# Kernel tuning notes

Hardware: AMD Instinct MI355X
Metric: run time of the kernel (lower is better)

The kernel has to match this reference:

```python
import jax, jax.numpy as jnp
import numpy as np

D = 256; HEADS = 8; DH = 32; LVLS = 3; PTS = 4; FF = 1024; FCD = 12544
SHAPES = ((100, 152), (50, 76), (25, 38))  # stride 8/16/32 maps for an 800x1216 image
INCH = (512, 1024, 2048)
N = 2; P_IMG = 1000


def sine_pos(h, w):
    # PositionEmbeddingSine, normalize=True, fully-valid mask
    eps = 1e-6; scale = 2.0 * np.pi
    y = jnp.cumsum(jnp.ones((h, w), jnp.float32), 0)
    x = jnp.cumsum(jnp.ones((h, w), jnp.float32), 1)
    y = y / (y[-1:, :] + eps) * scale
    x = x / (x[:, -1:] + eps) * scale
    dim_t = 10000.0 ** ((2.0 * (jnp.arange(128) // 2)).astype(jnp.float32) / 128.0)
    def inter(p):  # interleave sin/cos like torch.stack(...).flatten(3)
        return jnp.stack([jnp.sin(p[..., 0::2]), jnp.cos(p[..., 1::2])], -1).reshape(h, w, 128)
    return jnp.concatenate([inter(y[..., None] / dim_t), inter(x[..., None] / dim_t)], -1).reshape(h * w, D)


def bilinear(img, gx, gy):
    # F.grid_sample bilinear, align_corners=False, padding_mode='zeros'
    # img [C,H,W]; gx,gy in [-1,1] of any shape -> out [C, *gx.shape]
    C, H, W = img.shape
    x = ((gx + 1.0) * W - 1.0) * 0.5
    y = ((gy + 1.0) * H - 1.0) * 0.5
    x0 = jnp.floor(x); y0 = jnp.floor(y)
    wx = x - x0; wy = y - y0
    x0i = x0.astype(jnp.int32); y0i = y0.astype(jnp.int32)
    def g(xi, yi):
        ok = ((xi >= 0) & (xi < W) & (yi >= 0) & (yi < H)).astype(img.dtype)
        v = img[:, jnp.clip(yi, 0, H - 1), jnp.clip(xi, 0, W - 1)]
        return v * ok[None]
    return (g(x0i, y0i) * ((1 - wx) * (1 - wy))[None]
            + g(x0i + 1, y0i) * (wx * (1 - wy))[None]
            + g(x0i, y0i + 1) * ((1 - wx) * wy)[None]
            + g(x0i + 1, y0i + 1) * (wx * wy)[None])


def layernorm(x, g, b):
    mu = x.mean(-1, keepdims=True)
    var = ((x - mu) ** 2).mean(-1, keepdims=True)
    return (x - mu) / jnp.sqrt(var + 1e-5) * g + b


def _forward(feat0, feat1, feat2, point_coords, projw, projb, gng, gnb, level_embed,
             w_off, b_off, w_attn, b_attn, w_val, b_val, w_out, b_out,
             ln1_g, ln1_b, ln2_g, ln2_b, w_ff1, b_ff1, w_ff2, b_ff2, fc_w, fc_b):
    feats = (feat0, feat1, feat2)
    srcs = []; poss = []
    for l in range(LVLS):
        # input_proj: 1x1 conv + GroupNorm(32, 256)
        s = jnp.einsum('nchw,oc->nohw', feats[l], projw[l]) + projb[l][None, :, None, None]
        n, c, h, w = s.shape
        sg = s.reshape(n, 32, c // 32, h, w)
        mu = sg.mean((2, 3, 4), keepdims=True)
        var = ((sg - mu) ** 2).mean((2, 3, 4), keepdims=True)
        s = ((sg - mu) / jnp.sqrt(var + 1e-5)).reshape(n, c, h, w) * gng[l][None, :, None, None] + gnb[l][None, :, None, None]
        srcs.append(s.reshape(n, c, h * w).transpose(0, 2, 1))
        poss.append(sine_pos(h, w)[None] + level_embed[l][None, None, :])
    src = jnp.concatenate(srcs, 1)            # [N, Len, D]
    pos = jnp.concatenate(poss, 1)            # [1, Len, D] broadcast
    # reference points (valid_ratios == 1)
    refs = []
    for (h, w) in SHAPES:
        gy, gx = jnp.meshgrid((jnp.arange(h) + 0.5) / h, (jnp.arange(w) + 0.5) / w, indexing='ij')
        refs.append(jnp.stack([gx.ravel(), gy.ravel()], -1))
    ref = jnp.concatenate(refs, 0)            # [Len, 2] (x, y)
    Lq = src.shape[1]
    q = src + pos
    value = (src @ w_val.T + b_val).reshape(N, Lq, HEADS, DH)
    off = (q @ w_off.T + b_off).reshape(N, Lq, HEADS, LVLS, PTS, 2)
    aw = jax.nn.softmax((q @ w_attn.T + b_attn).reshape(N, Lq, HEADS, LVLS * PTS), -1).reshape(N, Lq, HEADS, LVLS, PTS)
    norm = jnp.array([[w, h] for (h, w) in SHAPES], jnp.float32)  # [L, 2] offset normalizer (W_, H_)
    locs = ref[None, :, None, None, None, :] + off / norm[None, None, None, :, None, :]  # [N,Lq,H,L,P,2]
    # MSDeformAttn core: per-level bilinear gather, accumulate weighted samples
    acc = jnp.zeros((N * HEADS, DH, Lq), src.dtype)
    start = 0
    for lvl, (h, w) in enumerate(SHAPES):
        v = value[:, start:start + h * w].transpose(0, 2, 3, 1).reshape(N * HEADS, DH, h, w)
        g = (2.0 * locs[:, :, :, lvl] - 1.0).transpose(0, 2, 1, 3, 4).reshape(N * HEADS, Lq, PTS, 2)
        s = jax.vmap(bilinear)(v, g[..., 0], g[..., 1])                 # [NH, DH, Lq, PTS]
        a = aw[:, :, :, lvl].transpose(0, 2, 1, 3).reshape(N * HEADS, 1, Lq, PTS)
        acc = acc + (s * a).sum(-1)
        start += h * w
    attn_out = acc.reshape(N, HEADS * DH, Lq).transpose(0, 2, 1) @ w_out.T + b_out
    x = layernorm(src + attn_out, ln1_g, ln1_b)
    ff = jax.nn.relu(x @ w_ff1.T + b_ff1) @ w_ff2.T + b_ff2
    x = layernorm(x + ff, ln2_g, ln2_b)
    # take level-0 tokens back to a feature map
    H0, W0 = SHAPES[0]
    mem = x.transpose(0, 2, 1)[:, :, :H0 * W0].reshape(N, D, H0, W0)
    # point_sample: grid_sample at 2*coords-1
    gpc = 2.0 * point_coords - 1.0
    pf = jax.vmap(bilinear)(mem, gpc[..., 0], gpc[..., 1])              # [N, D, P]
    pf = pf.transpose(0, 2, 1).reshape(N * P_IMG, D)
    # fc: Conv1d(256 -> 12544, k=1) + relu, then squeeze/permute
    return jax.nn.relu(pf @ fc_w.T + fc_b[None])


def setup_inputs() -> dict:
    key = jax.random.key(0)
    ki = iter(jax.random.split(key, 48))
    def rn(shape, scale):
        return jax.random.normal(next(ki), shape, jnp.float32) * scale
    d = {}
    d['feat0'] = jax.random.normal(next(ki), (N, 512, 100, 152), jnp.float32)
    d['feat1'] = jax.random.normal(next(ki), (N, 1024, 50, 76), jnp.float32)
    d['feat2'] = jax.random.normal(next(ki), (N, 2048, 25, 38), jnp.float32)
    d['point_coords'] = jax.random.uniform(next(ki), (N, P_IMG, 2), jnp.float32)
    d['gt_classes'] = jax.random.randint(next(ki), (N * P_IMG,), 0, 81)
    for l in range(LVLS):
        cin = INCH[l]
        d[f'proj{l}_w'] = rn((D, cin), 1.0 / np.sqrt(cin))
        d[f'proj{l}_b'] = jnp.zeros((D,), jnp.float32)
        d[f'gn{l}_g'] = jnp.ones((D,), jnp.float32)
        d[f'gn{l}_b'] = jnp.zeros((D,), jnp.float32)
    d['level_embed'] = rn((LVLS, D), 1.0)
    d['w_off'] = rn((HEADS * LVLS * PTS * 2, D), 0.01)
    d['b_off'] = rn((HEADS * LVLS * PTS * 2,), 0.2)
    d['w_attn'] = rn((HEADS * LVLS * PTS, D), 0.01)
    d['b_attn'] = jnp.zeros((HEADS * LVLS * PTS,), jnp.float32)
    d['w_val'] = rn((D, D), 1.0 / 16)
    d['b_val'] = jnp.zeros((D,), jnp.float32)
    d['w_out'] = rn((D, D), 1.0 / 16)
    d['b_out'] = jnp.zeros((D,), jnp.float32)
    d['ln1_g'] = jnp.ones((D,), jnp.float32); d['ln1_b'] = jnp.zeros((D,), jnp.float32)
    d['ln2_g'] = jnp.ones((D,), jnp.float32); d['ln2_b'] = jnp.zeros((D,), jnp.float32)
    d['w_ff1'] = rn((FF, D), 1.0 / 16); d['b_ff1'] = jnp.zeros((FF,), jnp.float32)
    d['w_ff2'] = rn((D, FF), 1.0 / 32); d['b_ff2'] = jnp.zeros((D,), jnp.float32)
    d['fc_w'] = rn((FCD, D), 1.0 / 16); d['fc_b'] = jnp.zeros((FCD,), jnp.float32)
    return d


def reference(feat0, feat1, feat2, point_coords, gt_classes,
              proj0_w, proj0_b, gn0_g, gn0_b, proj1_w, proj1_b, gn1_g, gn1_b,
              proj2_w, proj2_b, gn2_g, gn2_b, level_embed,
              w_off, b_off, w_attn, b_attn, w_val, b_val, w_out, b_out,
              ln1_g, ln1_b, ln2_g, ln2_b, w_ff1, b_ff1, w_ff2, b_ff2, fc_w, fc_b):
    out = _forward(feat0, feat1, feat2, point_coords,
                   (proj0_w, proj1_w, proj2_w), (proj0_b, proj1_b, proj2_b),
                   (gn0_g, gn1_g, gn2_g), (gn0_b, gn1_b, gn2_b), level_embed,
                   w_off, b_off, w_attn, b_attn, w_val, b_val, w_out, b_out,
                   ln1_g, ln1_b, ln2_g, ln2_b, w_ff1, b_ff1, w_ff2, b_ff2, fc_w, fc_b)
    return (out, gt_classes)
```

## Files before the change

### kernel.cpp

```cpp
#include <hip/hip_runtime.h>
#include <cstddef>
#include <cstdint>

#define D_MODEL 256
#define LQ 19950
#define NBATCH 2
#define NT (NBATCH*LQ)

typedef short  bf16x8 __attribute__((ext_vector_type(8)));
typedef float  f32x4  __attribute__((ext_vector_type(4)));
typedef unsigned short u16x8 __attribute__((ext_vector_type(8)));
typedef unsigned short u16x4 __attribute__((ext_vector_type(4)));
typedef _Float16 h16x2 __attribute__((ext_vector_type(2)));

__device__ __forceinline__ unsigned short f2b(float f) {
  unsigned u = __float_as_uint(f);
  u += 0x7fff + ((u >> 16) & 1);
  return (unsigned short)(u >> 16);
}
__device__ __forceinline__ float b2f(unsigned short s) {
  return __uint_as_float(((unsigned)s) << 16);
}
__device__ __forceinline__ bf16x8 pack8(float4 a, float4 b) {
  bf16x8 r;
  r[0]=(short)f2b(a.x); r[1]=(short)f2b(a.y); r[2]=(short)f2b(a.z); r[3]=(short)f2b(a.w);
  r[4]=(short)f2b(b.x); r[5]=(short)f2b(b.y); r[6]=(short)f2b(b.z); r[7]=(short)f2b(b.w);
  return r;
}

#if __has_builtin(__builtin_amdgcn_global_load_lds)
#define HAVE_GLL 1
__device__ __forceinline__ void gload16(const void* g, void* lds_base_uniform) {
  __builtin_amdgcn_global_load_lds(
      (const __attribute__((address_space(1))) void*)g,
      (__attribute__((address_space(3))) void*)lds_base_uniform, 16, 0, 0);
}
#else
#define HAVE_GLL 0
#endif

template<bool ABF, int BMODE, bool CBF, bool RELU, bool ROWBIAS>
__global__ __launch_bounds__(256) void mgemm(
    const void* __restrict__ Av, const void* __restrict__ Bv,
    const float* __restrict__ bias, void* __restrict__ Cv,
    int M, int N, int K, int lda, int ldb, long sB, long sC, int zShift)
{
  __shared__ unsigned short As[64][72];
  __shared__ unsigned short Bs[64][72];
  const int tid = threadIdx.x;
  const int n0 = blockIdx.x * 64, m0 = blockIdx.y * 64;
  const int zb = blockIdx.z;
  const int n_b = zb >> zShift;
  const int kBase = (zb & ((1 << zShift) - 1)) * K;
  const int lane = tid & 63;
  const int wave = tid >> 6;
  const int l15 = lane & 15, q = lane >> 4;
  const int m_off = (wave >> 1) * 32, n_off = (wave & 1) * 32;
  f32x4 acc[2][2] = {};

  for (int k0 = kBase; k0 < kBase + K; k0 += 64) {
    {
      int row = tid >> 2, kc = (tid & 3) * 8;
      int gm = m0 + row;
      bf16x8 v0 = (bf16x8)0, v1 = (bf16x8)0;
      if (gm < M) {
        if constexpr (ABF) {
          const unsigned short* A = (const unsigned short*)Av;
          v0 = *(const bf16x8*)&A[(size_t)gm*lda + k0 + kc];
          v1 = *(const bf16x8*)&A[(size_t)gm*lda + k0 + kc + 32];
        } else {
          const float* A = (const float*)Av;
          const float* p = &A[(size_t)gm*lda + k0 + kc];
          v0 = pack8(*(const float4*)p,      *(const float4*)(p+4));
          v1 = pack8(*(const float4*)(p+32), *(const float4*)(p+36));
        }
      }
      *(bf16x8*)&As[row][kc]    = v0;
      *(bf16x8*)&As[row][kc+32] = v1;
    }
    if constexpr (BMODE == 1) {
      const float* Bp = (const float*)Bv + (size_t)n_b * sB;
      int kr = tid >> 3, nc = (tid & 7) * 8;
      #pragma unroll
      for (int half = 0; half < 2; ++half) {
        int kk = kr + half*32;
        const float* p = &Bp[(size_t)(k0+kk)*ldb + n0 + nc];
        float v[8];
        if (n0 + nc + 7 < N) {
          float2 a0 = *(const float2*)p,     a1 = *(const float2*)(p+2);
          float2 a2 = *(const float2*)(p+4), a3 = *(const float2*)(p+6);
          v[0]=a0.x; v[1]=a0.y; v[2]=a1.x; v[3]=a1.y;
          v[4]=a2.x; v[5]=a2.y; v[6]=a3.x; v[7]=a3.y;
        } else {
          #pragma unroll
          for (int i=0;i<8;++i) v[i] = (n0+nc+i < N) ? p[i] : 0.f;
        }
        #pragma unroll
        for (int i=0;i<8;++i) Bs[nc+i][kk] = f2b(v[i]);
      }
    }
    __syncthreads();
    #pragma unroll
    for (int s = 0; s < 2; ++s) {
      bf16x8 a0 = *(const bf16x8*)&As[m_off      + l15][s*32 + q*8];
      bf16x8 a1 = *(const bf16x8*)&As[m_off + 16 + l15][s*32 + q*8];
      bf16x8 b0 = *(const bf16x8*)&Bs[n_off      + l15][s*32 + q*8];
      bf16x8 b1 = *(const bf16x8*)&Bs[n_off + 16 + l15][s*32 + q*8];
      acc[0][0] = __builtin_amdgcn_mfma_f32_16x16x32_bf16(a0, b0, acc[0][0], 0,0,0);
      acc[0][1] = __builtin_amdgcn_mfma_f32_16x16x32_bf16(a0, b1, acc[0][1], 0,0,0);
      acc[1][0] = __builtin_amdgcn_mfma_f32_16x16x32_bf16(a1, b0, acc[1][0], 0,0,0);
      acc[1][1] = __builtin_amdgcn_mfma_f32_16x16x32_bf16(a1, b1, acc[1][1], 0,0,0);
    }
    __syncthreads();
  }
  float* Cf = (float*)Cv + (size_t)zb * sC;
  unsigned short* Cb = (unsigned short*)Cv + (size_t)zb * sC;
  #pragma unroll
  for (int r = 0; r < 2; ++r) {
    #pragma unroll
    for (int c = 0; c < 2; ++c) {
      #pragma unroll
      for (int v = 0; v < 4; ++v) {
        int gm = m0 + m_off + r*16 + q*4 + v;
        int gn = n0 + n_off + c*16 + l15;
        if (gm < M && gn < N) {
          float o = acc[r][c][v];
          if (bias) o += ROWBIAS ? bias[gm] : bias[gn];
          if (RELU) o = fmaxf(o, 0.f);
          if constexpr (CBF) Cb[(size_t)gm*N + gn] = f2b(o);
          else               Cf[(size_t)gm*N + gn] = o;
        }
      }
    }
  }
}

__global__ __launch_bounds__(256) void proj_reduce2(
    const float* __restrict__ part, const float* __restrict__ bias,
    float* __restrict__ out, int HW, int S)
{
  int half = HW >> 1;
  int per_n = D_MODEL * half;
  int total = NBATCH * per_n;
  const float2* p2 = (const float2*)part;
  float2* o2 = (float2*)out;
  for (int i = blockIdx.x*256 + threadIdx.x; i < total; i += gridDim.x*256) {
    int n = i / per_n;
    int r = i - n*per_n;
    int o = r / half;
    int hw2 = r - o*half;
    float ax = 0.f, ay = 0.f;
    for (int s = 0; s < S; ++s) {
      float2 v = p2[((size_t)(n*S+s)*D_MODEL + o)*half + hw2];
      ax += v.x; ay += v.y;
    }
    float b = bias[o];
    o2[(size_t)o*HW + (size_t)n*half + hw2] = make_float2(ax+b, ay+b);
  }
}

template<bool CBF, bool RELU, bool RB>
__global__ __launch_bounds__(512) void gemm_bb(
    const unsigned short* __restrict__ A, const unsigned short* __restrict__ B,
    const float* __restrict__ bias, void* __restrict__ Cv,
    int M, int N, int K, int lda, int ldb)
{
  __shared__ unsigned short SA[8192];
  __shared__ unsigned short SB[8192];
  const int tid = threadIdx.x;
  const int lane = tid & 63, wave = tid >> 6;
  const int nwg = gridDim.x * gridDim.y;
  const int flat = blockIdx.y * gridDim.x + blockIdx.x;
  const int qn = nwg >> 3, rr = nwg & 7;
  const int xcd = flat & 7, lid = flat >> 3;
  const int swz = (xcd < rr ? xcd*(qn+1) : rr*(qn+1) + (xcd-rr)*qn) + lid;
  const int n0 = (swz % gridDim.x) * 128;
  const int m0 = (swz / gridDim.x) * 128;

  const int l15 = lane & 15, q = lane >> 4;
  const int m_off = (wave >> 2) * 64, n_off = (wave & 3) * 32;
  const int sr = lane >> 3;
  const int ssl = (lane & 7) ^ sr;
  const int rs = l15 & 7;
  f32x4 acc[4][2] = {};

  for (int k0 = 0; k0 < K; k0 += 64) {
    #pragma unroll
    for (int c = 0; c < 2; ++c) {
      int ch = wave*2 + c;
      const unsigned short* ga = A + (size_t)(m0 + ch*8 + sr)*lda + k0 + ssl*8;
      const unsigned short* gb = B + (size_t)(n0 + ch*8 + sr)*ldb + k0 + ssl*8;
#if HAVE_GLL
      gload16(ga, &SA[ch*512]);
      gload16(gb, &SB[ch*512]);
#else
      *(bf16x8*)&SA[ch*512 + lane*8] = *(const bf16x8*)ga;
      *(bf16x8*)&SB[ch*512 + lane*8] = *(const bf16x8*)gb;
#endif
    }
    __syncthreads();
    #pragma unroll
    for (int s = 0; s < 2; ++s) {
      int ps = ((s*4 + q) ^ rs) * 8;
      bf16x8 af[4], bfr[2];
      #pragma unroll
      for (int i = 0; i < 4; ++i)
        af[i] = *(const bf16x8*)&SA[(m_off + i*16 + l15)*64 + ps];
      #pragma unroll
      for (int j = 0; j < 2; ++j)
        bfr[j] = *(const bf16x8*)&SB[(n_off + j*16 + l15)*64 + ps];
      #pragma unroll
      for (int i = 0; i < 4; ++i)
        #pragma unroll
        for (int j = 0; j < 2; ++j)
          acc[i][j] = __builtin_amdgcn_mfma_f32_16x16x32_bf16(af[i], bfr[j], acc[i][j], 0,0,0);
    }
    __syncthreads();
  }

  float* Cf = (float*)Cv;
  unsigned short* Cb = (unsigned short*)Cv;
  #pragma unroll
  for (int i = 0; i < 4; ++i) {
    #pragma unroll
    for (int j = 0; j < 2; ++j) {
      #pragma unroll
      for (int v = 0; v < 4; ++v) {
        int gm = m0 + m_off + i*16 + q*4 + v;
        int gn = n0 + n_off + j*16 + l15;
        if (gm < M && gn < N) {
          float o = acc[i][j][v];
          if (bias) o += RB ? bias[gm] : bias[gn];
          if (RELU) o = fmaxf(o, 0.f);
          if constexpr (CBF) Cb[(size_t)gm*N + gn] = f2b(o);
          else               Cf[(size_t)gm*N + gn] = o;
        }
      }
    }
  }
}

template<bool CBF, bool RELU, bool RB>
__global__ __launch_bounds__(512) void gemm_wide(
    const unsigned short* __restrict__ A, const unsigned short* __restrict__ B,
    const float* __restrict__ bias, void* __restrict__ Cv,
    int M, int N, int K, int lda, int ldb)
{
  __shared__ unsigned short SA[8192];
  __shared__ unsigned short SB[16384];
  const int tid = threadIdx.x;
  const int lane = tid & 63, wave = tid >> 6;
  const int nwg = gridDim.x * gridDim.y;
  const int flat = blockIdx.y * gridDim.x + blockIdx.x;
  const int qn = nwg >> 3, rr = nwg & 7;
  const int xcd = flat & 7, lid = flat >> 3;
  const int swz = (xcd < rr ? xcd*(qn+1) : rr*(qn+1) + (xcd-rr)*qn) + lid;
  const int n0 = (swz % gridDim.x) * 256;
  const int m0 = (swz / gridDim.x) * 128;

  const int l15 = lane & 15, q = lane >> 4;
  const int m_off = (wave >> 2) * 64, n_off = (wave & 3) * 64;
  const int sr = lane >> 3;
  const int ssl = (lane & 7) ^ sr;
  const int rs = l15 & 7;
  f32x4 acc[4][4] = {};

  for (int k0 = 0; k0 < K; k0 += 64) {
    #pragma unroll
    for (int c = 0; c < 2; ++c) {
      int ch = wave*2 + c;
      const unsigned short* ga = A + (size_t)(m0 + ch*8 + sr)*lda + k0 + ssl*8;
#if HAVE_GLL
      gload16(ga, &SA[ch*512]);
#else
      *(bf16x8*)&SA[ch*512 + lane*8] = *(const bf16x8*)ga;
#endif
    }
    #pragma unroll
    for (int c = 0; c < 4; ++c) {
      int ch = wave*4 + c;
      const unsigned short* gb = B + (size_t)(n0 + ch*8 + sr)*ldb + k0 + ssl*8;
#if HAVE_GLL
      gload16(gb, &SB[ch*512]);
#else
      *(bf16x8*)&SB[ch*512 + lane*8] = *(const bf16x8*)gb;
#endif
    }
    __syncthreads();
    #pragma unroll
    for (int s = 0; s < 2; ++s) {
      int ps = ((s*4 + q) ^ rs) * 8;
      bf16x8 af[4], bfr[4];
      #pragma unroll
      for (int i = 0; i < 4; ++i)
        af[i] = *(const bf16x8*)&SA[(m_off + i*16 + l15)*64 + ps];
      #pragma unroll
      for (int j = 0; j < 4; ++j)
        bfr[j] = *(const bf16x8*)&SB[(n_off + j*16 + l15)*64 + ps];
      #pragma unroll
      for (int i = 0; i < 4; ++i)
        #pragma unroll
        for (int j = 0; j < 4; ++j)
          acc[i][j] = __builtin_amdgcn_mfma_f32_16x16x32_bf16(af[i], bfr[j], acc[i][j], 0,0,0);
    }
    __syncthreads();
  }

  float* Cf = (float*)Cv;
  unsigned short* Cb = (unsigned short*)Cv;
  #pragma unroll
  for (int i = 0; i < 4; ++i) {
    #pragma unroll
    for (int j = 0; j < 4; ++j) {
      #pragma unroll
      for (int v = 0; v < 4; ++v) {
        int gm = m0 + m_off + i*16 + q*4 + v;
        int gn = n0 + n_off + j*16 + l15;
        if (gm < M && gn < N) {
          float o = acc[i][j][v];
          if (bias) o += RB ? bias[gm] : bias[gn];
          if (RELU) o = fmaxf(o, 0.f);
          if constexpr (CBF) Cb[(size_t)gm*N + gn] = f2b(o);
          else               Cf[(size_t)gm*N + gn] = o;
        }
      }
    }
  }
}

__global__ __launch_bounds__(512) void gemm_vo(
    const unsigned short* __restrict__ Asrc, const unsigned short* __restrict__ Aq,
    const unsigned short* __restrict__ Bv,   const unsigned short* __restrict__ Bo,
    const float* __restrict__ bias_v, const float* __restrict__ bias_o,
    unsigned short* __restrict__ Cv, unsigned short* __restrict__ Co, int M)
{
  __shared__ unsigned short SA[8192];
  __shared__ unsigned short SB[8192];
  const int tid = threadIdx.x;
  const int lane = tid & 63, wave = tid >> 6;
  const int nwg = gridDim.x * gridDim.y;
  const int flat = blockIdx.y * gridDim.x + blockIdx.x;
  const int qn = nwg >> 3, rr = nwg & 7;
  const int xcd = flat & 7, lid = flat >> 3;
  const int swz = (xcd < rr ? xcd*(qn+1) : rr*(qn+1) + (xcd-rr)*qn) + lid;
  const int colid = swz % gridDim.x;
  const int m0 = (swz / gridDim.x) * 128;

  const unsigned short* A; const unsigned short* B;
  const float* bias; unsigned short* C; int N, n0; bool isv;
  if (colid < 2) { A = Asrc; B = Bv; bias = bias_v; C = Cv; N = 256; n0 = colid*128; isv = true; }
  else           { A = Aq;   B = Bo; bias = bias_o; C = Co; N = 288; n0 = (colid-2)*128; isv = false; }

  const int l15 = lane & 15, q = lane >> 4;
  const int m_off = (wave >> 2) * 64, n_off = (wave & 3) * 32;
  const int sr = lane >> 3;
  const int ssl = (lane & 7) ^ sr;
  const int rs = l15 & 7;
  f32x4 acc[4][2] = {};

  for (int k0 = 0; k0 < 256; k0 += 64) {
    #pragma unroll
    for (int c = 0; c < 2; ++c) {
      int ch = wave*2 + c;
      const unsigned short* ga = A + (size_t)(m0 + ch*8 + sr)*256 + k0 + ssl*8;
      const unsigned short* gb = B + (size_t)(n0 + ch*8 + sr)*256 + k0 + ssl*8;
#if HAVE_GLL
      gload16(ga, &SA[ch*512]);
      gload16(gb, &SB[ch*512]);
#else
      *(bf16x8*)&SA[ch*512 + lane*8] = *(const bf16x8*)ga;
      *(bf16x8*)&SB[ch*512 + lane*8] = *(const bf16x8*)gb;
#endif
    }
    __syncthreads();
    #pragma unroll
    for (int s = 0; s < 2; ++s) {
      int ps = ((s*4 + q) ^ rs) * 8;
      bf16x8 af[4], bfr[2];
      #pragma unroll
      for (int i = 0; i < 4; ++i)
        af[i] = *(const bf16x8*)&SA[(m_off + i*16 + l15)*64 + ps];
      #pragma unroll
      for (int j = 0; j < 2; ++j)
        bfr[j] = *(const bf16x8*)&SB[(n_off + j*16 + l15)*64 + ps];
      #pragma unroll
      for (int i = 0; i < 4; ++i)
        #pragma unroll
        for (int j = 0; j < 2; ++j)
          acc[i][j] = __builtin_amdgcn_mfma_f32_16x16x32_bf16(af[i], bfr[j], acc[i][j], 0,0,0);
    }
    __syncthreads();
  }

  #pragma unroll
  for (int i = 0; i < 4; ++i) {
    #pragma unroll
    for (int j = 0; j < 2; ++j) {
      #pragma unroll
      for (int v = 0; v < 4; ++v) {
        int gm = m0 + m_off + i*16 + q*4 + v;
        int gn = n0 + n_off + j*16 + l15;
        if (gm < M && gn < N) {
          float o = acc[i][j][v] + bias[gn];
          unsigned short bits;
          if (isv) { _Float16 hh = (_Float16)o; bits = *(unsigned short*)&hh; }
          else     { bits = f2b(o); }
          C[(size_t)gm*N + gn] = bits;
        }
      }
    }
  }
}

__global__ __launch_bounds__(256) void tconv(
    const float* __restrict__ feat, unsigned short* __restrict__ featT,
    int C, int HW)
{
  __shared__ float T[32][33];
  int hw0 = blockIdx.x*32, c0 = blockIdx.y*32, n = blockIdx.z;
  const float* base = feat + (size_t)n*C*HW;
  int tx = threadIdx.x & 31, ty = threadIdx.x >> 5;
  #pragma unroll
  for (int it=0; it<4; ++it) {
    int c = c0 + ty + it*8;
    int hw = hw0 + tx;
    T[ty+it*8][tx] = (hw < HW) ? base[(size_t)c*HW + hw] : 0.f;
  }
  __syncthreads();
  #pragma unroll
  for (int it=0; it<4; ++it) {
    int tl = ty + it*8;
    int tok = hw0 + tl;
    if (tok < HW) {
      featT[((size_t)n*HW + tok)*C + c0 + tx] = f2b(T[tx][tl]);
    }
  }
}

struct W9 { const float* src[9]; unsigned short* dst[9]; int nv[9]; };
__global__ __launch_bounds__(256) void wconv(W9 w)
{
  int s = blockIdx.y;
  const float4* src = (const float4*)w.src[s];
  unsigned short* dst = w.dst[s];
  int n = w.nv[s];
  for (int i = blockIdx.x*256 + threadIdx.x; i < n; i += gridDim.x*256) {
    float4 v = src[i];
    u16x4 o = { f2b(v.x), f2b(v.y), f2b(v.z), f2b(v.w) };
    *(u16x4*)(dst + (size_t)i*4) = o;
  }
}

__global__ __launch_bounds__(288) void biascat(
    const float* __restrict__ b_off, const float* __restrict__ b_attn,
    float* __restrict__ out)
{
  int i = threadIdx.x;
  out[i] = (i < 192) ? b_off[i] : b_attn[i - 192];
}

__global__ __launch_bounds__(256) void gn_partial2(
    const float* __restrict__ s2, float* __restrict__ partials, int HW)
{
  int g = blockIdx.x, n = blockIdx.y, c = blockIdx.z;
  int NHW = HW*2;
  int nvec2 = HW >> 1;
  int total = nvec2*8;
  float sum = 0.f, sq = 0.f;
  for (int j = c*256 + threadIdx.x; j < total; j += 2048) {
    int r = j / nvec2;
    int v = j - r*nvec2;
    const float2 x = *(const float2*)(s2 + (size_t)(g*8+r)*NHW + (size_t)n*HW + v*2);
    sum += x.x + x.y;
    sq  += x.x*x.x + x.y*x.y;
  }
  #pragma unroll
  for (int m=32;m;m>>=1){ sum += __shfl_xor(sum,m,64); sq += __shfl_xor(sq,m,64); }
  __shared__ float s1[4], s2s[4];
  int w = threadIdx.x >> 6;
  if ((threadIdx.x & 63) == 0) { s1[w]=sum; s2s[w]=sq; }
  __syncthreads();
  if (threadIdx.x == 0) {
    partials[(((size_t)n*32+g)*8 + c)*2]     = s1[0]+s1[1]+s1[2]+s1[3];
    partials[(((size_t)n*32+g)*8 + c)*2 + 1] = s2s[0]+s2s[1]+s2s[2]+s2s[3];
  }
}

__global__ __launch_bounds__(256) void gn_apply2(
    const float* __restrict__ s2, const float* __restrict__ partials,
    const float* __restrict__ gw, const float* __restrict__ gb,
    const float* __restrict__ le,
    float* __restrict__ src, unsigned short* __restrict__ srcbf,
    unsigned short* __restrict__ qb,
    int HW, int loff, int W, float invW, float invH2pi, float invW2pi)
{
  __shared__ float T[32][33];
  __shared__ float smu[4], srs[4];
  int tx = threadIdx.x & 31, ty = threadIdx.x >> 5;
  int hw0 = blockIdx.x*32, o0 = blockIdx.y*32, n = blockIdx.z;
  int NHW = HW*2;
  if (threadIdx.x < 4) {
    int g = (o0 >> 3) + threadIdx.x;
    float S = 0.f, Q = 0.f;
    #pragma unroll
    for (int c = 0; c < 8; ++c) {
      S += partials[(((size_t)n*32+g)*8 + c)*2];
      Q += partials[(((size_t)n*32+g)*8 + c)*2 + 1];
    }
    float inv = 1.f/(float)(8*HW);
    float mu = S*inv;
    float var = Q*inv - mu*mu;
    smu[threadIdx.x] = mu;
    srs[threadIdx.x] = rsqrtf(var + 1e-5f);
  }
  __syncthreads();
  #pragma unroll
  for (int it=0; it<4; ++it) {
    int ol = ty + it*8;
    int o = o0 + ol;
    int hw = hw0 + tx;
    float v = 0.f;
    if (hw < HW) {
      v = (s2[(size_t)o*NHW + (size_t)n*HW + hw] - smu[ol>>3])*srs[ol>>3]*gw[o] + gb[o];
    }
    T[ol][tx] = v;
  }
  __syncthreads();
  int d = o0 + tx;
  int m = (d & 127) >> 1;
  float invt = __expf((float)m * -0.14391156516f);
  float lev  = le[d];
  #pragma unroll
  for (int it=0; it<4; ++it) {
    int tl = ty + it*8;
    int tok = hw0 + tl;
    if (tok < HW) {
      size_t idx = ((size_t)n*LQ + loff + tok)*D_MODEL + d;
      float v = T[tx][tl];
      src[idx] = v;
      srcbf[idx] = f2b(v);
      int i = __float2int_rd(((float)tok + 0.5f) * invW);
      int j = tok - i*W;
      float ang = ((d < 128) ? (float)(i+1)*invH2pi : (float)(j+1)*invW2pi) * invt;
      float pe = (d & 1) ? __cosf(ang) : __sinf(ang);
      qb[idx] = f2b(v + pe + lev);
    }
  }
}

__global__ __launch_bounds__(256) void deform_sample(
    const unsigned short* __restrict__ value, const unsigned short* __restrict__ offaw,
    unsigned short* __restrict__ accb)
{
  int idx = blockIdx.x*256 + threadIdx.x;
  if (idx >= NT*8*4) return;
  int quarter = idx & 3;
  int h = (idx >> 2) & 7;
  int row = idx >> 5;
  int n = (row >= LQ) ? 1 : 0;
  int tok = row - n*LQ;

  float bxs0, bxs1, bxs2, bys0, bys1, bys2;
  if (tok < 15200) {
    int ti = tok/152, tj = tok - ti*152;
    float bx = tj + 0.5f, by = ti + 0.5f;
    bxs0 = bx - 0.5f;         bys0 = by - 0.5f;
    bxs1 = bx*0.5f - 0.5f;    bys1 = by*0.5f - 0.5f;
    bxs2 = bx*0.25f - 0.5f;   bys2 = by*0.25f - 0.5f;
  } else if (tok < 19000) {
    int hw = tok - 15200; int ti = hw/76, tj = hw - ti*76;
    float bx = tj + 0.5f, by = ti + 0.5f;
    bxs0 = bx*2.f - 0.5f;     bys0 = by*2.f - 0.5f;
    bxs1 = bx - 0.5f;         bys1 = by - 0.5f;
    bxs2 = bx*0.5f - 0.5f;    bys2 = by*0.5f - 0.5f;
  } else {
    int hw = tok - 19000; int ti = hw/38, tj = hw - ti*38;
    float bx = tj + 0.5f, by = ti + 0.5f;
    bxs0 = bx*4.f - 0.5f;     bys0 = by*4.f - 0.5f;
    bxs1 = bx*2.f - 0.5f;     bys1 = by*2.f - 0.5f;
    bxs2 = bx - 0.5f;         bys2 = by - 0.5f;
  }
  const float bxs[3] = {bxs0, bxs1, bxs2};
  const float bys[3] = {bys0, bys1, bys2};

  const unsigned short* offr = offaw + (size_t)row*288 + h*24;
  const unsigned short* awr  = offaw + (size_t)row*288 + 192 + h*12;
  float off[24];
  {
    u16x8 o0 = *(const u16x8*)offr;
    u16x8 o1 = *(const u16x8*)(offr+8);
    u16x8 o2 = *(const u16x8*)(offr+16);
    #pragma unroll
    for (int c=0;c<8;++c){ off[c]=b2f(o0[c]); off[8+c]=b2f(o1[c]); off[16+c]=b2f(o2[c]); }
  }
  float lg[12];
  {
    u16x4 a0 = *(const u16x4*)awr;
    u16x4 a1 = *(const u16x4*)(awr+4);
    u16x4 a2 = *(const u16x4*)(awr+8);
    #pragma unroll
    for (int c=0;c<4;++c){ lg[c]=b2f(a0[c]); lg[4+c]=b2f(a1[c]); lg[8+c]=b2f(a2[c]); }
  }
  float mx = -1e30f;
  #pragma unroll
  for (int i=0;i<12;++i) mx = fmaxf(mx, lg[i]);
  float ssum = 0.f;
  #pragma unroll
  for (int i=0;i<12;++i){ lg[i] = __expf(lg[i]-mx); ssum += lg[i]; }
  float sinv = 1.f/ssum;

  h16x2 acc2[4] = {};
  const int HH[3]={100,50,25}, WW[3]={152,76,38}, OO[3]={0,15200,19000};
  int chbase = h*32 + quarter*8;
  const _Float16* vhalf = (const _Float16*)value;
  #pragma unroll
  for (int lvl=0; lvl<3; ++lvl) {
    const int H=HH[lvl], W=WW[lvl], lo=OO[lvl];
    const _Float16* vbase = vhalf + ((size_t)(n*LQ + lo)*D_MODEL) + chbase;
    #pragma unroll
    for (int p=0; p<4; ++p) {
      float ox = off[lvl*8 + p*2];
      float oy = off[lvl*8 + p*2 + 1];
      float a  = lg[lvl*4 + p] * sinv;
      float x = bxs[lvl] + ox;
      float y = bys[lvl] + oy;
      float x0f = floorf(x), y0f = floorf(y);
      float wx = x - x0f, wy = y - y0f;
      int x0 = (int)x0f, y0 = (int)y0f;
      float w00 = (1.f-wx)*(1.f-wy)*a, w10 = wx*(1.f-wy)*a;
      float w01 = (1.f-wx)*wy*a,       w11 = wx*wy*a;
      if ((unsigned)x0 < (unsigned)(W-1) && (unsigned)y0 < (unsigned)(H-1)) {
        const h16x2* p00 = (const h16x2*)(vbase + (size_t)(y0*W + x0)*D_MODEL);
        const h16x2* p10 = (const h16x2*)(vbase + (size_t)(y0*W + x0 + 1)*D_MODEL);
        const h16x2* p01 = (const h16x2*)(vbase + (size_t)((y0+1)*W + x0)*D_MODEL);
        const h16x2* p11 = (const h16x2*)(vbase + (size_t)((y0+1)*W + x0 + 1)*D_MODEL);
        _Float16 h00 = (_Float16)w00, h10 = (_Float16)w10;
        _Float16 h01 = (_Float16)w01, h11 = (_Float16)w11;
        h16x2 wp00 = {h00,h00}, wp10 = {h10,h10}, wp01 = {h01,h01}, wp11 = {h11,h11};
        #pragma unroll
        for (int k=0;k<4;++k) {
          acc2[k] += wp00*p00[k];
          acc2[k] += wp10*p10[k];
          acc2[k] += wp01*p01[k];
          acc2[k] += wp11*p11[k];
        }
      } else {
        float tw[4] = { w00, w10, w01, w11 };
        #pragma unroll
        for (int t=0; t<4; ++t) {
          int xi = x0 + (t & 1), yi = y0 + (t >> 1);
          if (xi >= 0 && xi < W && yi >= 0 && yi < H) {
            _Float16 wh = (_Float16)tw[t];
            h16x2 wp = {wh, wh};
            const h16x2* vr = (const h16x2*)(vbase + (size_t)(yi*W + xi)*D_MODEL);
            #pragma unroll
            for (int k=0;k<4;++k) acc2[k] += wp*vr[k];
          }
        }
      }
    }
  }
  unsigned short* o = accb + (size_t)row*D_MODEL + chbase;
  u16x8 ov;
  #pragma unroll
  for (int k=0;k<4;++k) {
    ov[k*2]   = f2b((float)acc2[k][0]);
    ov[k*2+1] = f2b((float)acc2[k][1]);
  }
  *(u16x8*)o = ov;
}

template<bool EMITBF>
__global__ __launch_bounds__(256) void ln_add(
    const float* __restrict__ A, const float* __restrict__ B,
    const float* __restrict__ g, const float* __restrict__ b,
    float* __restrict__ out, unsigned short* __restrict__ outbf, int rows)
{
  int wid = (blockIdx.x * 256 + threadIdx.x) >> 6;
  int lane = threadIdx.x & 63;
  if (wid >= rows) return;
  size_t base = (size_t)wid * D_MODEL;
  float4 va = *(const float4*)&A[base + lane*4];
  float4 vb = *(const float4*)&B[base + lane*4];
  float v[4] = {va.x+vb.x, va.y+vb.y, va.z+vb.z, va.w+vb.w};
  float s = v[0]+v[1]+v[2]+v[3];
  #pragma unroll
  for (int m=32; m; m>>=1) s += __shfl_xor(s, m, 64);
  float mu = s * (1.f/256.f);
  float qq = 0.f;
  #pragma unroll
  for (int i=0;i<4;++i){ float d=v[i]-mu; qq += d*d; }
  #pragma unroll
  for (int m=32; m; m>>=1) qq += __shfl_xor(qq, m, 64);
  float rstd = rsqrtf(qq*(1.f/256.f) + 1e-5f);
  float o[4];
  #pragma unroll
  for (int i=0;i<4;++i){
    int d = lane*4+i;
    o[i] = (v[i]-mu)*rstd*g[d] + b[d];
  }
  *(float4*)&out[base + lane*4] = make_float4(o[0],o[1],o[2],o[3]);
  if constexpr (EMITBF) {
    u16x4 ob = { f2b(o[0]), f2b(o[1]), f2b(o[2]), f2b(o[3]) };
    *(u16x4*)&outbf[base + lane*4] = ob;
  }
}

__global__ __launch_bounds__(256) void point_sample(
    const float* __restrict__ x2, const float* __restrict__ pc,
    unsigned short* __restrict__ pf)
{
  int pidx = blockIdx.x;
  int n = pidx / 1000;
  float px = pc[(size_t)pidx*2], py = pc[(size_t)pidx*2+1];
  float x = ((2.f*px)*152.f - 1.f)*0.5f;
  float y = ((2.f*py)*100.f - 1.f)*0.5f;
  float x0f=floorf(x), y0f=floorf(y);
  float wx=x-x0f, wy=y-y0f;
  int x0=(int)x0f, y0=(int)y0f;
  int d = threadIdx.x;
  float accv = 0.f;
  #pragma unroll
  for (int t=0;t<4;++t) {
    int xi = x0 + (t&1), yi = y0 + (t>>1);
    float w = ((t&1)?wx:(1.f-wx)) * ((t>>1)?wy:(1.f-wy));
    if (xi>=0 && xi<152 && yi>=0 && yi<100) {
      accv += w * x2[((size_t)(n*LQ + yi*152 + xi))*D_MODEL + d];
    }
  }
  pf[(size_t)pidx*D_MODEL + d] = f2b(accv);
}

__global__ void copy_gt(const int* __restrict__ gt, float* __restrict__ out, int nels)
{
  int i = blockIdx.x*256 + threadIdx.x;
  if (i < nels) out[i] = (float)gt[i];
}

extern "C" void kernel_launch(void* const* d_in, const int* in_sizes, int n_in,
                              void* d_out, int out_size, void* d_ws, size_t ws_size,
                              hipStream_t stream)
{
  const float* feat[3]  = {(const float*)d_in[0], (const float*)d_in[1], (const float*)d_in[2]};
  const float* pc       = (const float*)d_in[3];
  const int*   gt       = (const int*)d_in[4];
  const float* projw[3] = {(const float*)d_in[5],  (const float*)d_in[9],  (const float*)d_in[13]};
  const float* projb[3] = {(const float*)d_in[6],  (const float*)d_in[10], (const float*)d_in[14]};
  const float* gng[3]   = {(const float*)d_in[7],  (const float*)d_in[11], (const float*)d_in[15]};
  const float* gnb[3]   = {(const float*)d_in[8],  (const float*)d_in[12], (const float*)d_in[16]};
  const float* level_embed = (const float*)d_in[17];
  const float* w_off  = (const float*)d_in[18];
  const float* b_off  = (const float*)d_in[19];
  const float* w_attn = (const float*)d_in[20];
  const float* b_attn = (const float*)d_in[21];
  const float* w_val  = (const float*)d_in[22];
  const float* b_val  = (const float*)d_in[23];
  const float* w_out  = (const float*)d_in[24];
  const float* b_out  = (const float*)d_in[25];
  const float* ln1g   = (const float*)d_in[26];
  const float* ln1b   = (const float*)d_in[27];
  const float* ln2g   = (const float*)d_in[28];
  const float* ln2b   = (const float*)d_in[29];
  const float* wff1   = (const float*)d_in[30];
  const float* bff1   = (const float*)d_in[31];
  const float* wff2   = (const float*)d_in[32];
  const float* bff2   = (const float*)d_in[33];
  const float* fcw    = (const float*)d_in[34];
  const float* fcb    = (const float*)d_in[35];

  float* ws    = (float*)d_ws;
  float* s_tmp = ws;
  unsigned short* q_b     = (unsigned short*)(s_tmp + 10214400);
  unsigned short* value_b = q_b + 10214400;
  float* srcb  = (float*)(value_b + 10214400);
  float* xreg  = srcb + 10214400;
  unsigned short* offaw   = (unsigned short*)(xreg + 10214400);
  unsigned short* wbf     = offaw + 11491200;
  float* partials = (float*)(wbf + 4333568);
  float* boffaw   = partials + 1024;

  unsigned short* wv_bf  = wbf;
  unsigned short* wof_bf = wbf + 65536;
  unsigned short* wat_bf = wbf + 114688;
  unsigned short* wou_bf = wbf + 139264;
  unsigned short* wf1_bf = wbf + 204800;
  unsigned short* wf2_bf = wbf + 466944;
  unsigned short* wfc_bf = wbf + 729088;
  unsigned short* wp0_bf = wbf + 3940352;
  unsigned short* wp1_bf = wbf + 4071424;

  unsigned short* featT = q_b;
  float* kpart = (float*)offaw;
  unsigned short* src_bf = (unsigned short*)xreg;
  unsigned short* acc_b = q_b;
  unsigned short* xb_bf = offaw;
  unsigned short* hbuf  = (unsigned short*)s_tmp;
  unsigned short* pf    = value_b;
  float* ybuf = srcb;
  float* x2   = s_tmp;

  W9 w9;
  w9.src[0]=w_val;    w9.dst[0]=wv_bf;  w9.nv[0]=65536/4;
  w9.src[1]=w_off;    w9.dst[1]=wof_bf; w9.nv[1]=49152/4;
  w9.src[2]=w_attn;   w9.dst[2]=wat_bf; w9.nv[2]=24576/4;
  w9.src[3]=w_out;    w9.dst[3]=wou_bf; w9.nv[3]=65536/4;
  w9.src[4]=wff1;     w9.dst[4]=wf1_bf; w9.nv[4]=262144/4;
  w9.src[5]=wff2;     w9.dst[5]=wf2_bf; w9.nv[5]=262144/4;
  w9.src[6]=fcw;      w9.dst[6]=wfc_bf; w9.nv[6]=3211264/4;
  w9.src[7]=projw[0]; w9.dst[7]=wp0_bf; w9.nv[7]=131072/4;
  w9.src[8]=projw[1]; w9.dst[8]=wp1_bf; w9.nv[8]=262144/4;
  wconv<<<dim3(512, 9), 256, 0, stream>>>(w9);
  biascat<<<1, 288, 0, stream>>>(b_off, b_attn, boffaw);

  const float PI2 = 6.28318530717958647692f;
  {
    tconv<<<dim3(475, 16, 2), 256, 0, stream>>>(feat[0], featT, 512, 15200);
    gemm_wide<false,false,true><<<dim3(119, 2), 512, 0, stream>>>(
        wp0_bf, featT, projb[0], s_tmp, 256, 30400, 512, 512, 512);
    gn_partial2<<<dim3(32, 2, 8), 256, 0, stream>>>(s_tmp, partials, 15200);
    gn_apply2<<<dim3(475, 8, 2), 256, 0, stream>>>(
        s_tmp, partials, gng[0], gnb[0], level_embed, srcb, src_bf, q_b,
        15200, 0, 152, 1.0f/152.f, PI2/(100.f+1e-6f), PI2/(152.f+1e-6f));
  }
  {
    tconv<<<dim3(119, 32, 2), 256, 0, stream>>>(feat[1], featT, 1024, 3800);
    gemm_wide<false,false,true><<<dim3(30, 2), 512, 0, stream>>>(
        wp1_bf, featT, projb[1], s_tmp, 256, 7600, 1024, 1024, 1024);
    gn_partial2<<<dim3(32, 2, 8), 256, 0, stream>>>(s_tmp, partials, 3800);
    gn_apply2<<<dim3(119, 8, 2), 256, 0, stream>>>(
        s_tmp, partials, gng[1], gnb[1], level_embed + 256, srcb, src_bf, q_b,
        3800, 15200, 76, 1.0f/76.f, PI2/(50.f+1e-6f), PI2/(76.f+1e-6f));
  }
  {
    mgemm<false,1,false,false,true><<<dim3(15, 4, 8), 256, 0, stream>>>(
        projw[2], feat[2], nullptr, kpart, D_MODEL, 950, 512, 2048, 950,
        (long)2048*950, (long)D_MODEL*950, 2);
    int total2 = NBATCH * D_MODEL * (950 >> 1);
    int gr = (total2 + 255) / 256; if (gr > 2048) gr = 2048;
    proj_reduce2<<<gr, 256, 0, stream>>>(kpart, projb[2], s_tmp, 950, 4);
    gn_partial2<<<dim3(32, 2, 8), 256, 0, stream>>>(s_tmp, partials, 950);
    gn_apply2<<<dim3(30, 8, 2), 256, 0, stream>>>(
        s_tmp, partials, gng[2], gnb[2], level_embed + 512, srcb, src_bf, q_b,
        950, 19000, 38, 1.0f/38.f, PI2/(25.f+1e-6f), PI2/(38.f+1e-6f));
  }

  int gm128 = (NT + 127) / 128;
  gemm_vo<<<dim3(5, gm128), 512, 0, stream>>>(
      src_bf, q_b, wv_bf, wof_bf, b_val, boffaw, value_b, offaw, NT);

  deform_sample<<<(NT*8*4 + 255)/256, 256, 0, stream>>>(value_b, offaw, acc_b);

  gemm_bb<false,false,false><<<dim3(2, gm128), 512, 0, stream>>>(
      acc_b, wou_bf, b_out, s_tmp, NT, 256, 256, 256, 256);
  ln_add<true><<<(NT+3)/4, 256, 0, stream>>>(srcb, s_tmp, ln1g, ln1b, xreg, xb_bf, NT);

  gemm_wide<true,true,false><<<dim3(4, gm128), 512, 0, stream>>>(
      xb_bf, wf1_bf, bff1, hbuf, NT, 1024, 256, 256, 256);
  gemm_bb<false,false,false><<<dim3(2, gm128), 512, 0, stream>>>(
      hbuf, wf2_bf, bff2, ybuf, NT, 256, 1024, 1024, 1024);

  ln_add<false><<<(NT+3)/4, 256, 0, stream>>>(xreg, ybuf, ln2g, ln2b, x2, nullptr, NT);

  point_sample<<<2000, 256, 0, stream>>>(x2, pc, pf);
  gemm_wide<false,true,false><<<dim3(49, (2000+127)/128), 512, 0, stream>>>(
      pf, wfc_bf, fcb, (float*)d_out, 2000, 12544, 256, 256, 256);
  copy_gt<<<8, 256, 0, stream>>>(gt, (float*)d_out + (size_t)2000*12544, 2000);
}
```

Measured before the change: 480.7 us.

## Fuse residual add and LayerNorm into full-width output GEMM epilogues

Replaces the generic wide GEMM with a 128x256-tile GEMM whose tile covers the whole 256-wide model row. Its epilogue adds bias and the residual, reduces row mean and variance through shuffles and shared memory, and writes the normalized output, optionally also in bf16. This removes the two separate ln_add kernels and the fp32 intermediate round trips for the out-projection and FF2 results. The other former wide-GEMM calls now use gemm_bb with doubled grid x, and buffer aliasing is adjusted. Variance is computed as E[x^2]-mu^2, which is slightly less numerically stable, and the fused kernel launches only one block column, so there is less parallelism per GEMM.

After: 525.8 us. +9.4%, slower.

```diff
diff --git a/kernel.cpp b/kernel.cpp
--- a/kernel.cpp
+++ b/kernel.cpp
@@ -240,29 +240,30 @@
   }
 }
 
-template<bool CBF, bool RELU, bool RB>
-__global__ __launch_bounds__(512) void gemm_wide(
+template<bool EMITBF>
+__global__ __launch_bounds__(512) void gemm_ln(
     const unsigned short* __restrict__ A, const unsigned short* __restrict__ B,
-    const float* __restrict__ bias, void* __restrict__ Cv,
-    int M, int N, int K, int lda, int ldb)
+    const float* __restrict__ bias, const float* __restrict__ R,
+    const float* __restrict__ g, const float* __restrict__ b,
+    float* __restrict__ out, unsigned short* __restrict__ outbf,
+    int M, int K, int lda, int ldb)
 {
   __shared__ unsigned short SA[8192];
   __shared__ unsigned short SB[16384];
   const int tid = threadIdx.x;
   const int lane = tid & 63, wave = tid >> 6;
-  const int nwg = gridDim.x * gridDim.y;
-  const int flat = blockIdx.y * gridDim.x + blockIdx.x;
-  const int qn = nwg >> 3, rr = nwg & 7;
+  const int nwg = gridDim.y;
+  const int flat = blockIdx.y;
+  const int qn = nwg >> 3, rrm = nwg & 7;
   const int xcd = flat & 7, lid = flat >> 3;
-  const int swz = (xcd < rr ? xcd*(qn+1) : rr*(qn+1) + (xcd-rr)*qn) + lid;
-  const int n0 = (swz % gridDim.x) * 256;
-  const int m0 = (swz / gridDim.x) * 128;
+  const int swz = (xcd < rrm ? xcd*(qn+1) : rrm*(qn+1) + (xcd-rrm)*qn) + lid;
+  const int m0 = swz * 128;
 
   const int l15 = lane & 15, q = lane >> 4;
   const int m_off = (wave >> 2) * 64, n_off = (wave & 3) * 64;
   const int sr = lane >> 3;
   const int ssl = (lane & 7) ^ sr;
-  const int rs = l15 & 7;
+  const int rsk = l15 & 7;
   f32x4 acc[4][4] = {};
 
   for (int k0 = 0; k0 < K; k0 += 64) {
@@ -279,7 +280,7 @@
     #pragma unroll
     for (int c = 0; c < 4; ++c) {
       int ch = wave*4 + c;
-      const unsigned short* gb = B + (size_t)(n0 + ch*8 + sr)*ldb + k0 + ssl*8;
+      const unsigned short* gb = B + (size_t)(ch*8 + sr)*ldb + k0 + ssl*8;
 #if HAVE_GLL
       gload16(gb, &SB[ch*512]);
 #else
@@ -289,7 +290,7 @@
     __syncthreads();
     #pragma unroll
     for (int s = 0; s < 2; ++s) {
-      int ps = ((s*4 + q) ^ rs) * 8;
+      int ps = ((s*4 + q) ^ rsk) * 8;
       bf16x8 af[4], bfr[4];
       #pragma unroll
       for (int i = 0; i < 4; ++i)
@@ -306,22 +307,78 @@
     __syncthreads();
   }
 
-  float* Cf = (float*)Cv;
-  unsigned short* Cb = (unsigned short*)Cv;
+  float srow[4][4], qrow[4][4];
   #pragma unroll
   for (int i = 0; i < 4; ++i) {
     #pragma unroll
-    for (int j = 0; j < 4; ++j) {
+    for (int v = 0; v < 4; ++v) {
+      int gm = m0 + m_off + i*16 + q*4 + v;
+      float sr_ = 0.f, qr_ = 0.f;
+      #pragma unroll
+      for (int j = 0; j < 4; ++j) {
+        int gn = n_off + j*16 + l15;
+        float o = acc[i][j][v] + bias[gn];
+        if (gm < M) o += R[(size_t)gm*D_MODEL + gn];
+        acc[i][j][v] = o;
+        sr_ += o; qr_ += o*o;
+      }
+      srow[i][v] = sr_; qrow[i][v] = qr_;
+    }
+  }
+  #pragma unroll
+  for (int m = 1; m < 16; m <<= 1) {
+    #pragma unroll
+    for (int i = 0; i < 4; ++i)
       #pragma unroll
       for (int v = 0; v < 4; ++v) {
-        int gm = m0 + m_off + i*16 + q*4 + v;
-        int gn = n0 + n_off + j*16 + l15;
-        if (gm < M && gn < N) {
-          float o = acc[i][j][v];
-          if (bias) o += RB ? bias[gm] : bias[gn];
-          if (RELU) o = fmaxf(o, 0.f);
-          if constexpr (CBF) Cb[(size_t)gm*N + gn] = f2b(o);
-          else               Cf[(size_t)gm*N + gn] = o;
+        srow[i][v] += __shfl_xor(srow[i][v], m, 64);
+        qrow[i][v] += __shfl_xor(qrow[i][v], m, 64);
+      }
+  }
+  float* red  = (float*)SA;
+  float* rmu  = red + 1024;
+  float* rrsd = red + 1152;
+  int wgrp = wave & 3;
+  if (l15 == 0) {
+    #pragma unroll
+    for (int i = 0; i < 4; ++i)
+      #pragma unroll
+      for (int v = 0; v < 4; ++v) {
+        int lr = m_off + i*16 + q*4 + v;
+        red[lr*4 + wgrp]       = srow[i][v];
+        red[512 + lr*4 + wgrp] = qrow[i][v];
+      }
+  }
+  __syncthreads();
+  if (wgrp == 0 && l15 == 0) {
+    #pragma unroll
+    for (int i = 0; i < 4; ++i)
+      #pragma unroll
+      for (int v = 0; v < 4; ++v) {
+        int lr = m_off + i*16 + q*4 + v;
+        float S = red[lr*4] + red[lr*4+1] + red[lr*4+2] + red[lr*4+3];
+        float Q = red[512+lr*4] + red[512+lr*4+1] + red[512+lr*4+2] + red[512+lr*4+3];
+        float mu = S * (1.f/256.f);
+        float var = Q * (1.f/256.f) - mu*mu;
+        rmu[lr]  = mu;
+        rrsd[lr] = rsqrtf(var + 1e-5f);
+      }
+  }
+  __syncthreads();
+  #pragma unroll
+  for (int i = 0; i < 4; ++i) {
+    #pragma unroll
+    for (int v = 0; v < 4; ++v) {
+      int lr = m_off + i*16 + q*4 + v;
+      int gm = m0 + lr;
+      if (gm < M) {
+        float mu = rmu[lr], rsd = rrsd[lr];
+        #pragma unroll
+        for (int j = 0; j < 4; ++j) {
+          int gn = n_off + j*16 + l15;
+          float o = (acc[i][j][v] - mu) * rsd * g[gn] + b[gn];
+          out[(size_t)gm*D_MODEL + gn] = o;
+          if constexpr (EMITBF) outbf[(size_t)gm*D_MODEL + gn] = f2b(o);
         }
       }
     }
@@ -670,42 +727,6 @@
   *(u16x8*)o = ov;
 }
 
-template<bool EMITBF>
-__global__ __launch_bounds__(256) void ln_add(
-    const float* __restrict__ A, const float* __restrict__ B,
-    const float* __restrict__ g, const float* __restrict__ b,
-    float* __restrict__ out, unsigned short* __restrict__ outbf, int rows)
-{
-  int wid = (blockIdx.x * 256 + threadIdx.x) >> 6;
-  int lane = threadIdx.x & 63;
-  if (wid >= rows) return;
-  size_t base = (size_t)wid * D_MODEL;
-  float4 va = *(const float4*)&A[base + lane*4];
-  float4 vb = *(const float4*)&B[base + lane*4];
-  float v[4] = {va.x+vb.x, va.y+vb.y, va.z+vb.z, va.w+vb.w};
-  float s = v[0]+v[1]+v[2]+v[3];
-  #pragma unroll
-  for (int m=32; m; m>>=1) s += __shfl_xor(s, m, 64);
-  float mu = s * (1.f/256.f);
-  float qq = 0.f;
-  #pragma unroll
-  for (int i=0;i<4;++i){ float d=v[i]-mu; qq += d*d; }
-  #pragma unroll
-  for (int m=32; m; m>>=1) qq += __shfl_xor(qq, m, 64);
-  float rstd = rsqrtf(qq*(1.f/256.f) + 1e-5f);
-  float o[4];
-  #pragma unroll
-  for (int i=0;i<4;++i){
-    int d = lane*4+i;
-    o[i] = (v[i]-mu)*rstd*g[d] + b[d];
-  }
-  *(float4*)&out[base + lane*4] = make_float4(o[0],o[1],o[2],o[3]);
-  if constexpr (EMITBF) {
-    u16x4 ob = { f2b(o[0]), f2b(o[1]), f2b(o[2]), f2b(o[3]) };
-    *(u16x4*)&outbf[base + lane*4] = ob;
-  }
-}
-
 __global__ __launch_bounds__(256) void point_sample(
     const float* __restrict__ x2, const float* __restrict__ pc,
     unsigned short* __restrict__ pf)
@@ -789,15 +810,14 @@
   unsigned short* wp0_bf = wbf + 3940352;
   unsigned short* wp1_bf = wbf + 4071424;
 
-  unsigned short* featT = q_b;
+  unsigned short* featT = value_b;
   float* kpart = (float*)offaw;
   unsigned short* src_bf = (unsigned short*)xreg;
   unsigned short* acc_b = q_b;
   unsigned short* xb_bf = offaw;
   unsigned short* hbuf  = (unsigned short*)s_tmp;
   unsigned short* pf    = value_b;
-  float* ybuf = srcb;
-  float* x2   = s_tmp;
+  float* x2 = srcb;
 
   W9 w9;
   w9.src[0]=w_val;    w9.dst[0]=wv_bf;  w9.nv[0]=65536/4;
@@ -815,7 +835,7 @@
   const float PI2 = 6.28318530717958647692f;
   {
     tconv<<<dim3(475, 16, 2), 256, 0, stream>>>(feat[0], featT, 512, 15200);
-    gemm_wide<false,false,true><<<dim3(119, 2), 512, 0, stream>>>(
+    gemm_bb<false,false,true><<<dim3(238, 2), 512, 0, stream>>>(
         wp0_bf, featT, projb[0], s_tmp, 256, 30400, 512, 512, 512);
     gn_partial2<<<dim3(32, 2, 8), 256, 0, stream>>>(s_tmp, partials, 15200);
     gn_apply2<<<dim3(475, 8, 2), 256, 0, stream>>>(
@@ -824,7 +844,7 @@
   }
   {
     tconv<<<dim3(119, 32, 2), 256, 0, stream>>>(feat[1], featT, 1024, 3800);
-    gemm_wide<false,false,true><<<dim3(30, 2), 512, 0, stream>>>(
+    gemm_bb<false,false,true><<<dim3(60, 2), 512, 0, stream>>>(
         wp1_bf, featT, projb[1], s_tmp, 256, 7600, 1024, 1024, 1024);
     gn_partial2<<<dim3(32, 2, 8), 256, 0, stream>>>(s_tmp, partials, 3800);
     gn_apply2<<<dim3(119, 8, 2), 256, 0, stream>>>(
@@ -850,19 +870,16 @@
 
   deform_sample<<<(NT*8*4 + 255)/256, 256, 0, stream>>>(value_b, offaw, acc_b);
 
-  gemm_bb<false,false,false><<<dim3(2, gm128), 512, 0, stream>>>(
-      acc_b, wou_bf, b_out, s_tmp, NT, 256, 256, 256, 256);
-  ln_add<true><<<(NT+3)/4, 256, 0, stream>>>(srcb, s_tmp, ln1g, ln1b, xreg, xb_bf, NT);
-
-  gemm_wide<true,true,false><<<dim3(4, gm128), 512, 0, stream>>>(
+  gemm_ln<true><<<dim3(1, gm128), 512, 0, stream>>>(
+      acc_b, wou_bf, b_out, srcb, ln1g, ln1b, xreg, xb_bf, NT, 256, 256, 256);
+
+  gemm_bb<true,true,false><<<dim3(8, gm128), 512, 0, stream>>>(
       xb_bf, wf1_bf, bff1, hbuf, NT, 1024, 256, 256, 256);
-  gemm_bb<false,false,false><<<dim3(2, gm128), 512, 0, stream>>>(
-      hbuf, wf2_bf, bff2, ybuf, NT, 256, 1024, 1024, 1024);
-
-  ln_add<false><<<(NT+3)/4, 256, 0, stream>>>(xreg, ybuf, ln2g, ln2b, x2, nullptr, NT);
+  gemm_ln<false><<<dim3(1, gm128), 512, 0, stream>>>(
+      hbuf, wf2_bf, bff2, xreg, ln2g, ln2b, x2, nullptr, NT, 1024, 1024, 1024);
 
   point_sample<<<2000, 256, 0, stream>>>(x2, pc, pf);
-  gemm_wide<false,true,false><<<dim3(49, (2000+127)/128), 512, 0, stream>>>(
+  gemm_bb<false,true,false><<<dim3(98, (2000+127)/128), 512, 0, stream>>>(
       pf, wfc_bf, fcb, (float*)d_out, 2000, 12544, 256, 256, 256);
   copy_gt<<<8, 256, 0, stream>>>(gt, (float*)d_out + (size_t)2000*12544, 2000);
 }
```
